# Kernel tuning notes

Measured on AMD Instinct MI355X. Metric: run time of the kernel, lower is better.

The kernel has to match this reference:

```python
import jax, jax.numpy as jnp
import numpy as np

N_NODES = 65536
IN_FEAT = 512
OUT_FEAT = 256
N_REL = 3
N_EDGES = 500000
NEG_SLOPE = 0.2  # DGL GATConv default
EPS = 1e-9


def setup_inputs() -> dict:
    key = jax.random.key(0)
    ks = jax.random.split(key, 7)
    h = jax.random.normal(ks[0], (N_NODES, IN_FEAT), dtype=jnp.float32)
    # Glorot-ish scaling keeps attention logits in a sane range
    W = jax.random.normal(ks[1], (N_REL, IN_FEAT, OUT_FEAT), dtype=jnp.float32) / np.sqrt(IN_FEAT)
    attn_l = jax.random.normal(ks[2], (N_REL, OUT_FEAT), dtype=jnp.float32) / np.sqrt(OUT_FEAT)
    attn_r = jax.random.normal(ks[3], (N_REL, OUT_FEAT), dtype=jnp.float32) / np.sqrt(OUT_FEAT)
    b = jnp.zeros((N_REL, OUT_FEAT), dtype=jnp.float32)
    src = jax.random.randint(ks[4], (N_REL, N_EDGES), 0, N_NODES, dtype=jnp.int32)
    dst = jax.random.randint(ks[5], (N_REL, N_EDGES), 0, N_NODES, dtype=jnp.int32)
    return {"h": h, "W": W, "attn_l": attn_l, "attn_r": attn_r, "b": b, "src": src, "dst": dst}


def _gat_relation(h, W_r, al_r, ar_r, b_r, src_r, dst_r):
    n = h.shape[0]
    z = h @ W_r                                  # [N, F_out] dense projection
    el = z @ al_r                                # [N] per-node left logit
    er = z @ ar_r                                # [N] per-node right logit
    e = jax.nn.leaky_relu(el[src_r] + er[dst_r], NEG_SLOPE)  # [E]
    # edge_softmax over incoming edges of each destination node
    m = jax.ops.segment_max(e, dst_r, num_segments=n)        # [N]
    w = jnp.exp(e - m[dst_r])                                # [E]
    denom = jax.ops.segment_sum(w, dst_r, num_segments=n)    # [N]
    alpha = w / (denom[dst_r] + EPS)                         # [E]
    out = jax.ops.segment_sum(alpha[:, None] * z[src_r], dst_r, num_segments=n)
    return out + b_r


def reference(h, W, attn_l, attn_r, b, src, dst):
    n_rel = W.shape[0]
    out = jnp.zeros((h.shape[0], W.shape[2]), dtype=h.dtype)
    # HeteroGraphConv default aggregate='sum' over relations; num_heads=1 then squeeze
    for r in range(n_rel):
        out = out + _gat_relation(h, W[r], attn_l[r], attn_r[r], b[r], src[r], dst[r])
    return out
```

## Files before the change

### kernel.cpp

```cpp
#include <hip/hip_runtime.h>
#include <hip/hip_bf16.h>
#include <cstdint>
#include <cstddef>

#define N_NODES 65536
#define IN_FEAT 512
#define OUT_FEAT 256
#define N_REL 3
#define TOT_EDGES (N_REL * 500000)
#define N_EDGES 500000
#define NEG_SLOPE 0.2f
#define EPS_F 1e-9f
#define BK 64

typedef __bf16 bf16x8 __attribute__((ext_vector_type(8)));
typedef float f32x4 __attribute__((ext_vector_type(4)));

__device__ __forceinline__ void async16(const void* g, void* l) {
    __builtin_amdgcn_global_load_lds(
        (const __attribute__((address_space(1))) unsigned int*)g,
        (__attribute__((address_space(3))) unsigned int*)l, 16, 0, 0);
}

__global__ __launch_bounds__(256) void kPrep(
    const float* __restrict__ W, const float* __restrict__ h,
    __bf16* __restrict__ Wt, __bf16* __restrict__ hb,
    float* __restrict__ el, float* __restrict__ er, int* __restrict__ head,
    int useHb) {
    __shared__ float tile[64][65];
    const int b = blockIdx.x;
    const int t = threadIdx.x;
    if (b < 768) {
        int i = b * 256 + t;
        el[i] = 0.f;
        er[i] = 0.f;
        head[i] = -1;
    } else if (b < 864) {
        int b2 = b - 768;
        int r = b2 >> 5;
        int kt = (b2 >> 2) & 7;
        int nt = b2 & 3;
        int k0 = kt * 64, n0 = nt * 64;
        int trow = t >> 6, tcol = t & 63;
        const float* Wr = W + (size_t)r * IN_FEAT * OUT_FEAT;
#pragma unroll
        for (int p = 0; p < 16; p++) {
            int k = p * 4 + trow;
            tile[k][tcol] = Wr[(size_t)(k0 + k) * OUT_FEAT + n0 + tcol];
        }
        __syncthreads();
        __bf16* Wtr = Wt + (size_t)r * OUT_FEAT * IN_FEAT;
#pragma unroll
        for (int p = 0; p < 16; p++) {
            int n = p * 4 + trow;
            Wtr[(size_t)(n0 + n) * IN_FEAT + k0 + tcol] = (__bf16)tile[tcol][n];
        }
    } else if (useHb) {
        size_t i = (size_t)(b - 864) * 256 + t;
        const float4* src = (const float4*)h + i * 2;
        float4 v0 = src[0], v1 = src[1];
        bf16x8 w;
        w[0] = (__bf16)v0.x; w[1] = (__bf16)v0.y; w[2] = (__bf16)v0.z; w[3] = (__bf16)v0.w;
        w[4] = (__bf16)v1.x; w[5] = (__bf16)v1.y; w[6] = (__bf16)v1.z; w[7] = (__bf16)v1.w;
        *(bf16x8*)(hb + i * 8) = w;
    }
}

__global__ __launch_bounds__(256, 3) void kGemmA(
    const __bf16* __restrict__ hb, const __bf16* __restrict__ Wt,
    const float* __restrict__ attn_l, const float* __restrict__ attn_r,
    __bf16* __restrict__ z, float* __restrict__ el, float* __restrict__ er) {
    __shared__ __bf16 Al[128 * BK];
    __shared__ __bf16 Bl[128 * BK];
    const int r = blockIdx.z;
    const int t = threadIdx.x;
    const int lane = t & 63;
    const int wave = t >> 6;
    const int wm = wave >> 1, wn = wave & 1;
    const int colL = lane & 15, quad = lane >> 4;
    const int m_base = blockIdx.y * 128;
    const int n_base = blockIdx.x * 128;

    const __bf16* WtR = Wt + (size_t)r * OUT_FEAT * IN_FEAT + (size_t)n_base * IN_FEAT;

    f32x4 acc[4][4];
#pragma unroll
    for (int mt = 0; mt < 4; mt++)
#pragma unroll
        for (int nt = 0; nt < 4; nt++) acc[mt][nt] = (f32x4){0.f, 0.f, 0.f, 0.f};

    for (int k0 = 0; k0 < IN_FEAT; k0 += BK) {
        if (k0) __syncthreads();
#pragma unroll
        for (int i = 0; i < 4; i++) {
            int s = i * 256 + t;
            int n = s >> 3, cp = s & 7, cs = cp ^ (n & 7);
            const __bf16* g = WtR + (size_t)n * IN_FEAT + k0 + cs * 8;
            __bf16* l = Bl + (size_t)(i * 256 + (wave << 6)) * 8;
            async16(g, l);
        }
#pragma unroll
        for (int i = 0; i < 4; i++) {
            int s = i * 256 + t;
            int row = s >> 3, cp = s & 7, cs = cp ^ (row & 7);
            const __bf16* g = hb + (size_t)(m_base + row) * IN_FEAT + k0 + cs * 8;
            __bf16* l = Al + (size_t)(i * 256 + (wave << 6)) * 8;
            async16(g, l);
        }
        __syncthreads();
#pragma unroll
        for (int kk = 0; kk < 2; kk++) {
            const int cbase = kk * 4 + quad;
            bf16x8 af[4], bfr[4];
#pragma unroll
            for (int mt = 0; mt < 4; mt++) {
                int row = wm * 64 + mt * 16 + colL;
                int cp = cbase ^ (row & 7);
                af[mt] = *(const bf16x8*)(Al + (size_t)((row << 3) + cp) * 8);
            }
#pragma unroll
            for (int nt = 0; nt < 4; nt++) {
                int n = wn * 64 + nt * 16 + colL;
                int cp = cbase ^ (n & 7);
                bfr[nt] = *(const bf16x8*)(Bl + (size_t)((n << 3) + cp) * 8);
            }
#pragma unroll
            for (int mt = 0; mt < 4; mt++)
#pragma unroll
                for (int nt = 0; nt < 4; nt++)
                    acc[mt][nt] = __builtin_amdgcn_mfma_f32_16x16x32_bf16(
                        af[mt], bfr[nt], acc[mt][nt], 0, 0, 0);
        }
    }

    const float* alv = attn_l + r * OUT_FEAT;
    const float* arv = attn_r + r * OUT_FEAT;
    __bf16* zr = z + (size_t)r * N_NODES * OUT_FEAT;
    float elp[4][4], erp[4][4];
#pragma unroll
    for (int mt = 0; mt < 4; mt++)
#pragma unroll
        for (int q = 0; q < 4; q++) { elp[mt][q] = 0.f; erp[mt][q] = 0.f; }
#pragma unroll
    for (int mt = 0; mt < 4; mt++) {
#pragma unroll
        for (int nt = 0; nt < 4; nt++) {
            int c = n_base + wn * 64 + nt * 16 + colL;
            float al = alv[c], ar = arv[c];
#pragma unroll
            for (int q = 0; q < 4; q++) {
                float v = acc[mt][nt][q];
                int row = m_base + wm * 64 + mt * 16 + quad * 4 + q;
                zr[(size_t)row * OUT_FEAT + c] = (__bf16)v;
                elp[mt][q] += v * al;
                erp[mt][q] += v * ar;
            }
        }
    }
#pragma unroll
    for (int mt = 0; mt < 4; mt++)
#pragma unroll
        for (int q = 0; q < 4; q++) {
#pragma unroll
            for (int off = 1; off < 16; off <<= 1) {
                elp[mt][q] += __shfl_xor(elp[mt][q], off, 64);
                erp[mt][q] += __shfl_xor(erp[mt][q], off, 64);
            }
        }
    if (colL == 0) {
#pragma unroll
        for (int mt = 0; mt < 4; mt++)
#pragma unroll
            for (int q = 0; q < 4; q++) {
                int row = m_base + wm * 64 + mt * 16 + quad * 4 + q;
                atomicAdd(el + r * N_NODES + row, elp[mt][q]);
                atomicAdd(er + r * N_NODES + row, erp[mt][q]);
            }
    }
}

__global__ __launch_bounds__(256) void kGemmC(
    const float* __restrict__ h, const __bf16* __restrict__ Wt,
    const float* __restrict__ attn_l, const float* __restrict__ attn_r,
    __bf16* __restrict__ z, float* __restrict__ el, float* __restrict__ er) {
    __shared__ __bf16 Al[128 * BK];
    __shared__ __bf16 Bl[256 * BK];
    const int r = blockIdx.y;
    const int t = threadIdx.x;
    const int lane = t & 63;
    const int wave = t >> 6;
    const int wm = wave >> 1, wn = wave & 1;
    const int colL = lane & 15, quad = lane >> 4;
    const int m_base = blockIdx.x * 128;
    const __bf16* WtR = Wt + (size_t)r * OUT_FEAT * IN_FEAT;

    f32x4 acc[4][8];
#pragma unroll
    for (int mt = 0; mt < 4; mt++)
#pragma unroll
        for (int nt = 0; nt < 8; nt++) acc[mt][nt] = (f32x4){0.f, 0.f, 0.f, 0.f};

    for (int k0 = 0; k0 < IN_FEAT; k0 += BK) {
        if (k0) __syncthreads();
#pragma unroll
        for (int i = 0; i < 8; i++) {
            int s = i * 256 + t;
            int n = s >> 3, cp = s & 7, cs = cp ^ (n & 7);
            const __bf16* g = WtR + (size_t)n * IN_FEAT + k0 + cs * 8;
            __bf16* l = Bl + (size_t)(i * 256 + (wave << 6)) * 8;
            async16(g, l);
        }
#pragma unroll
        for (int i = 0; i < 4; i++) {
            int s = i * 256 + t;
            int row = s >> 3, cp = s & 7, cs = cp ^ (row & 7);
            const float* g = h + (size_t)(m_base + row) * IN_FEAT + k0 + cs * 8;
            float4 v0 = ((const float4*)g)[0];
            float4 v1 = ((const float4*)g)[1];
            bf16x8 w;
            w[0] = (__bf16)v0.x; w[1] = (__bf16)v0.y; w[2] = (__bf16)v0.z; w[3] = (__bf16)v0.w;
            w[4] = (__bf16)v1.x; w[5] = (__bf16)v1.y; w[6] = (__bf16)v1.z; w[7] = (__bf16)v1.w;
            *(bf16x8*)(Al + (size_t)s * 8) = w;
        }
        __syncthreads();
#pragma unroll
        for (int kk = 0; kk < 2; kk++) {
            const int cbase = kk * 4 + quad;
            bf16x8 af[4], bfr[8];
#pragma unroll
            for (int mt = 0; mt < 4; mt++) {
                int row = wm * 64 + mt * 16 + colL;
                int cp = cbase ^ (row & 7);
                af[mt] = *(const bf16x8*)(Al + (size_t)((row << 3) + cp) * 8);
            }
#pragma unroll
            for (int nt = 0; nt < 8; nt++) {
                int n = wn * 128 + nt * 16 + colL;
                int cp = cbase ^ (n & 7);
                bfr[nt] = *(const bf16x8*)(Bl + (size_t)((n << 3) + cp) * 8);
            }
#pragma unroll
            for (int mt = 0; mt < 4; mt++)
#pragma unroll
                for (int nt = 0; nt < 8; nt++)
                    acc[mt][nt] = __builtin_amdgcn_mfma_f32_16x16x32_bf16(
                        af[mt], bfr[nt], acc[mt][nt], 0, 0, 0);
        }
    }
    const float* alv = attn_l + r * OUT_FEAT;
    const float* arv = attn_r + r * OUT_FEAT;
    __bf16* zr = z + (size_t)r * N_NODES * OUT_FEAT;
    float elp[4][4], erp[4][4];
#pragma unroll
    for (int mt = 0; mt < 4; mt++)
#pragma unroll
        for (int q = 0; q < 4; q++) { elp[mt][q] = 0.f; erp[mt][q] = 0.f; }
#pragma unroll
    for (int mt = 0; mt < 4; mt++) {
#pragma unroll
        for (int nt = 0; nt < 8; nt++) {
            int c = wn * 128 + nt * 16 + colL;
            float al = alv[c], ar = arv[c];
#pragma unroll
            for (int q = 0; q < 4; q++) {
                float v = acc[mt][nt][q];
                int row = m_base + wm * 64 + mt * 16 + quad * 4 + q;
                zr[(size_t)row * OUT_FEAT + c] = (__bf16)v;
                elp[mt][q] += v * al;
                erp[mt][q] += v * ar;
            }
        }
    }
#pragma unroll
    for (int mt = 0; mt < 4; mt++)
#pragma unroll
        for (int q = 0; q < 4; q++) {
#pragma unroll
            for (int off = 1; off < 16; off <<= 1) {
                elp[mt][q] += __shfl_xor(elp[mt][q], off, 64);
                erp[mt][q] += __shfl_xor(erp[mt][q], off, 64);
            }
        }
    if (colL == 0) {
#pragma unroll
        for (int mt = 0; mt < 4; mt++)
#pragma unroll
            for (int q = 0; q < 4; q++) {
                int row = m_base + wm * 64 + mt * 16 + quad * 4 + q;
                atomicAdd(el + r * N_NODES + row, elp[mt][q]);
                atomicAdd(er + r * N_NODES + row, erp[mt][q]);
            }
    }
}

__global__ void kLink(const int* __restrict__ dst, const int* __restrict__ srcArr,
                      int* __restrict__ head, int2* __restrict__ next2) {
    int i = blockIdx.x * blockDim.x + threadIdx.x;
    if (i >= TOT_EDGES) return;
    int r = i / N_EDGES;
    int d = dst[i];
    int prev = atomicExch(head + r * N_NODES + d, i);
    next2[i] = make_int2(prev, srcArr[i]);
}

__global__ __launch_bounds__(192) void kAgg(
    const __bf16* __restrict__ z, const int* __restrict__ head,
    const int2* __restrict__ next2,
    const float* __restrict__ el, const float* __restrict__ er,
    const float* __restrict__ bias, float* __restrict__ out) {
    __shared__ float cm[6][256];
    const int t = threadIdx.x;
    const int wv = t >> 6;
    const int lane = t & 63;
    const int half = lane >> 5;
    const int l = lane & 31;
    const int hw = wv * 2 + half;
    const int nl = (hw >= 3) ? 1 : 0;
    const int r = hw - nl * 3;
    const int node = blockIdx.x * 2 + nl;
    const int idx = r * N_NODES + node;

    const float erv = er[idx];
    const float* elr = el + r * N_NODES;
    const uint4* zrel = (const uint4*)(z + (size_t)r * N_NODES * OUT_FEAT);

    float p0 = 0.f, p1 = 0.f, p2 = 0.f, p3 = 0.f;
    float p4 = 0.f, p5 = 0.f, p6 = 0.f, p7 = 0.f;
    float wsum = 0.f;
    int cur = head[idx];
    while (cur >= 0) {
        int2 ns = next2[cur];
        int s = ns.y;
        float x = elr[s] + erv;
        x = x > 0.f ? x : NEG_SLOPE * x;
        float w = __expf(x);
        uint4 v = zrel[(size_t)s * 32 + l];
        wsum += w;
        p0 += w * __uint_as_float(v.x << 16);
        p1 += w * __uint_as_float(v.x & 0xFFFF0000u);
        p2 += w * __uint_as_float(v.y << 16);
        p3 += w * __uint_as_float(v.y & 0xFFFF0000u);
        p4 += w * __uint_as_float(v.z << 16);
        p5 += w * __uint_as_float(v.z & 0xFFFF0000u);
        p6 += w * __uint_as_float(v.w << 16);
        p7 += w * __uint_as_float(v.w & 0xFFFF0000u);
        cur = ns.x;
    }
    float invd = 1.f / (wsum + EPS_F);
    float* cr = &cm[hw][l * 8];
    *(float4*)cr       = make_float4(p0 * invd, p1 * invd, p2 * invd, p3 * invd);
    *(float4*)(cr + 4) = make_float4(p4 * invd, p5 * invd, p6 * invd, p7 * invd);
    __syncthreads();

    if (r == 0) {
        const int c = l * 8;
        const float* r0 = &cm[nl * 3 + 0][c];
        const float* r1 = &cm[nl * 3 + 1][c];
        const float* r2 = &cm[nl * 3 + 2][c];
        const float* b0 = bias + c;
        const float* b1 = bias + OUT_FEAT + c;
        const float* b2 = bias + 2 * OUT_FEAT + c;
        float f0 = r0[0] + r1[0] + r2[0] + b0[0] + b1[0] + b2[0];
        float f1 = r0[1] + r1[1] + r2[1] + b0[1] + b1[1] + b2[1];
        float f2 = r0[2] + r1[2] + r2[2] + b0[2] + b1[2] + b2[2];
        float f3 = r0[3] + r1[3] + r2[3] + b0[3] + b1[3] + b2[3];
        float f4 = r0[4] + r1[4] + r2[4] + b0[4] + b1[4] + b2[4];
        float f5 = r0[5] + r1[5] + r2[5] + b0[5] + b1[5] + b2[5];
        float f6 = r0[6] + r1[6] + r2[6] + b0[6] + b1[6] + b2[6];
        float f7 = r0[7] + r1[7] + r2[7] + b0[7] + b1[7] + b2[7];
        float* orow = out + (size_t)node * OUT_FEAT + c;
        *(float4*)orow       = make_float4(f0, f1, f2, f3);
        *(float4*)(orow + 4) = make_float4(f4, f5, f6, f7);
    }
}

extern "C" void kernel_launch(void* const* d_in, const int* in_sizes, int n_in,
                              void* d_out, int out_size, void* d_ws, size_t ws_size,
                              hipStream_t stream) {
    const float* h      = (const float*)d_in[0];
    const float* W      = (const float*)d_in[1];
    const float* attn_l = (const float*)d_in[2];
    const float* attn_r = (const float*)d_in[3];
    const float* bias   = (const float*)d_in[4];
    const int*   src    = (const int*)d_in[5];
    const int*   dst    = (const int*)d_in[6];
    float* out = (float*)d_out;
    char* ws = (char*)d_ws;

    const bool useHb = ws_size >= (size_t)190000000;
    size_t off_b = 0;
    auto alloc = [&](size_t bytes) {
        size_t o = off_b;
        off_b = (off_b + bytes + 255) & ~(size_t)255;
        return o;
    };
    size_t oZ    = alloc((size_t)N_REL * N_NODES * OUT_FEAT * 2);
    size_t oHB   = useHb ? alloc((size_t)N_NODES * IN_FEAT * 2) : 0;
    size_t oWT   = alloc((size_t)N_REL * OUT_FEAT * IN_FEAT * 2);
    size_t oEL   = alloc((size_t)N_REL * N_NODES * 4);
    size_t oER   = alloc((size_t)N_REL * N_NODES * 4);
    size_t oHEAD = alloc((size_t)N_REL * N_NODES * 4);
    size_t oNEXT = alloc((size_t)TOT_EDGES * 8);

    __bf16* z    = (__bf16*)(ws + oZ);
    __bf16* hb   = (__bf16*)(ws + oHB);
    __bf16* Wt   = (__bf16*)(ws + oWT);
    float*  el   = (float*)(ws + oEL);
    float*  er   = (float*)(ws + oER);
    int*    head = (int*)(ws + oHEAD);
    int2*   next2 = (int2*)(ws + oNEXT);

    kPrep<<<17248, 256, 0, stream>>>(W, h, Wt, hb, el, er, head, useHb ? 1 : 0);
    kLink<<<(TOT_EDGES + 255) / 256, 256, 0, stream>>>(dst, src, head, next2);
    if (useHb) {
        kGemmA<<<dim3(2, 512, 3), 256, 0, stream>>>(hb, Wt, attn_l, attn_r, z, el, er);
    } else {
        kGemmC<<<dim3(N_NODES / 128, N_REL), 256, 0, stream>>>(h, Wt, attn_l, attn_r, z, el, er);
    }
    kAgg<<<N_NODES / 2, 192, 0, stream>>>(z, head, next2, el, er, bias, out);
}
```

Measured before the change: 527.5 us.

## Drop bf16 h staging, XCD-aware GEMM scheduling, and interleave two node chains in aggregation

Removes the separate fp32-to-bf16 conversion pass over h and always uses the full-N GEMM that reads fp32 h directly. Blocks are remapped so each XCD handles a contiguous band of rows across all three relations, so the same h rows are shared in cache. The aggregation kernel now walks two destination nodes' linked lists at once per half-wave, giving more independent memory loads in flight to hide gather latency. The cost is more registers and divergence in the aggregation loop and an fp32 load-and-convert path inside the GEMM.

```diff
diff --git a/kernel.cpp b/kernel.cpp
--- a/kernel.cpp
+++ b/kernel.cpp
@@ -23,10 +23,9 @@
 }
 
 __global__ __launch_bounds__(256) void kPrep(
-    const float* __restrict__ W, const float* __restrict__ h,
-    __bf16* __restrict__ Wt, __bf16* __restrict__ hb,
-    float* __restrict__ el, float* __restrict__ er, int* __restrict__ head,
-    int useHb) {
+    const float* __restrict__ W,
+    __bf16* __restrict__ Wt,
+    float* __restrict__ el, float* __restrict__ er, int* __restrict__ head) {
     __shared__ float tile[64][65];
     const int b = blockIdx.x;
     const int t = threadIdx.x;
@@ -35,7 +34,7 @@
         el[i] = 0.f;
         er[i] = 0.f;
         head[i] = -1;
-    } else if (b < 864) {
+    } else {
         int b2 = b - 768;
         int r = b2 >> 5;
         int kt = (b2 >> 2) & 7;
@@ -55,143 +54,28 @@
             int n = p * 4 + trow;
             Wtr[(size_t)(n0 + n) * IN_FEAT + k0 + tcol] = (__bf16)tile[tcol][n];
         }
-    } else if (useHb) {
-        size_t i = (size_t)(b - 864) * 256 + t;
-        const float4* src = (const float4*)h + i * 2;
-        float4 v0 = src[0], v1 = src[1];
-        bf16x8 w;
-        w[0] = (__bf16)v0.x; w[1] = (__bf16)v0.y; w[2] = (__bf16)v0.z; w[3] = (__bf16)v0.w;
-        w[4] = (__bf16)v1.x; w[5] = (__bf16)v1.y; w[6] = (__bf16)v1.z; w[7] = (__bf16)v1.w;
-        *(bf16x8*)(hb + i * 8) = w;
-    }
-}
-
-__global__ __launch_bounds__(256, 3) void kGemmA(
-    const __bf16* __restrict__ hb, const __bf16* __restrict__ Wt,
+    }
+}
+
+__global__ __launch_bounds__(256, 2) void kGemm(
+    const float* __restrict__ h, const __bf16* __restrict__ Wt,
     const float* __restrict__ attn_l, const float* __restrict__ attn_r,
     __bf16* __restrict__ z, float* __restrict__ el, float* __restrict__ er) {
     __shared__ __bf16 Al[128 * BK];
-    __shared__ __bf16 Bl[128 * BK];
-    const int r = blockIdx.z;
+    __shared__ __bf16 Bl[256 * BK];
+    const int bid = blockIdx.x;
+    const int xcd = bid & 7;
+    const int slot = bid >> 3;
+    const int mt6 = slot / 3;
+    const int r = slot - mt6 * 3;
+    const int m_base = (xcd * 64 + mt6) * 128;
+
     const int t = threadIdx.x;
     const int lane = t & 63;
     const int wave = t >> 6;
     const int wm = wave >> 1, wn = wave & 1;
     const int colL = lane & 15, quad = lane >> 4;
-    const int m_base = blockIdx.y * 128;
-    const int n_base = blockIdx.x * 128;
-
-    const __bf16* WtR = Wt + (size_t)r * OUT_FEAT * IN_FEAT + (size_t)n_base * IN_FEAT;
-
-    f32x4 acc[4][4];
-#pragma unroll
-    for (int mt = 0; mt < 4; mt++)
-#pragma unroll
-        for (int nt = 0; nt < 4; nt++) acc[mt][nt] = (f32x4){0.f, 0.f, 0.f, 0.f};
-
-    for (int k0 = 0; k0 < IN_FEAT; k0 += BK) {
-        if (k0) __syncthreads();
-#pragma unroll
-        for (int i = 0; i < 4; i++) {
-            int s = i * 256 + t;
-            int n = s >> 3, cp = s & 7, cs = cp ^ (n & 7);
-            const __bf16* g = WtR + (size_t)n * IN_FEAT + k0 + cs * 8;
-            __bf16* l = Bl + (size_t)(i * 256 + (wave << 6)) * 8;
-            async16(g, l);
-        }
-#pragma unroll
-        for (int i = 0; i < 4; i++) {
-            int s = i * 256 + t;
-            int row = s >> 3, cp = s & 7, cs = cp ^ (row & 7);
-            const __bf16* g = hb + (size_t)(m_base + row) * IN_FEAT + k0 + cs * 8;
-            __bf16* l = Al + (size_t)(i * 256 + (wave << 6)) * 8;
-            async16(g, l);
-        }
-        __syncthreads();
-#pragma unroll
-        for (int kk = 0; kk < 2; kk++) {
-            const int cbase = kk * 4 + quad;
-            bf16x8 af[4], bfr[4];
-#pragma unroll
-            for (int mt = 0; mt < 4; mt++) {
-                int row = wm * 64 + mt * 16 + colL;
-                int cp = cbase ^ (row & 7);
-                af[mt] = *(const bf16x8*)(Al + (size_t)((row << 3) + cp) * 8);
-            }
-#pragma unroll
-            for (int nt = 0; nt < 4; nt++) {
-                int n = wn * 64 + nt * 16 + colL;
-                int cp = cbase ^ (n & 7);
-                bfr[nt] = *(const bf16x8*)(Bl + (size_t)((n << 3) + cp) * 8);
-            }
-#pragma unroll
-            for (int mt = 0; mt < 4; mt++)
-#pragma unroll
-                for (int nt = 0; nt < 4; nt++)
-                    acc[mt][nt] = __builtin_amdgcn_mfma_f32_16x16x32_bf16(
-                        af[mt], bfr[nt], acc[mt][nt], 0, 0, 0);
-        }
-    }
-
-    const float* alv = attn_l + r * OUT_FEAT;
-    const float* arv = attn_r + r * OUT_FEAT;
-    __bf16* zr = z + (size_t)r * N_NODES * OUT_FEAT;
-    float elp[4][4], erp[4][4];
-#pragma unroll
-    for (int mt = 0; mt < 4; mt++)
-#pragma unroll
-        for (int q = 0; q < 4; q++) { elp[mt][q] = 0.f; erp[mt][q] = 0.f; }
-#pragma unroll
-    for (int mt = 0; mt < 4; mt++) {
-#pragma unroll
-        for (int nt = 0; nt < 4; nt++) {
-            int c = n_base + wn * 64 + nt * 16 + colL;
-            float al = alv[c], ar = arv[c];
-#pragma unroll
-            for (int q = 0; q < 4; q++) {
-                float v = acc[mt][nt][q];
-                int row = m_base + wm * 64 + mt * 16 + quad * 4 + q;
-                zr[(size_t)row * OUT_FEAT + c] = (__bf16)v;
-                elp[mt][q] += v * al;
-                erp[mt][q] += v * ar;
-            }
-        }
-    }
-#pragma unroll
-    for (int mt = 0; mt < 4; mt++)
-#pragma unroll
-        for (int q = 0; q < 4; q++) {
-#pragma unroll
-            for (int off = 1; off < 16; off <<= 1) {
-                elp[mt][q] += __shfl_xor(elp[mt][q], off, 64);
-                erp[mt][q] += __shfl_xor(erp[mt][q], off, 64);
-            }
-        }
-    if (colL == 0) {
-#pragma unroll
-        for (int mt = 0; mt < 4; mt++)
-#pragma unroll
-            for (int q = 0; q < 4; q++) {
-                int row = m_base + wm * 64 + mt * 16 + quad * 4 + q;
-                atomicAdd(el + r * N_NODES + row, elp[mt][q]);
-                atomicAdd(er + r * N_NODES + row, erp[mt][q]);
-            }
-    }
-}
-
-__global__ __launch_bounds__(256) void kGemmC(
-    const float* __restrict__ h, const __bf16* __restrict__ Wt,
-    const float* __restrict__ attn_l, const float* __restrict__ attn_r,
-    __bf16* __restrict__ z, float* __restrict__ el, float* __restrict__ er) {
-    __shared__ __bf16 Al[128 * BK];
-    __shared__ __bf16 Bl[256 * BK];
-    const int r = blockIdx.y;
-    const int t = threadIdx.x;
-    const int lane = t & 63;
-    const int wave = t >> 6;
-    const int wm = wave >> 1, wn = wave & 1;
-    const int colL = lane & 15, quad = lane >> 4;
-    const int m_base = blockIdx.x * 128;
+
     const __bf16* WtR = Wt + (size_t)r * OUT_FEAT * IN_FEAT;
 
     f32x4 acc[4][8];
@@ -247,6 +131,7 @@
                         af[mt], bfr[nt], acc[mt][nt], 0, 0, 0);
         }
     }
+
     const float* alv = attn_l + r * OUT_FEAT;
     const float* arv = attn_r + r * OUT_FEAT;
     __bf16* zr = z + (size_t)r * N_NODES * OUT_FEAT;
@@ -308,7 +193,7 @@
     const int2* __restrict__ next2,
     const float* __restrict__ el, const float* __restrict__ er,
     const float* __restrict__ bias, float* __restrict__ out) {
-    __shared__ float cm[6][256];
+    __shared__ float cm[12][256];
     const int t = threadIdx.x;
     const int wv = t >> 6;
     const int lane = t & 63;
@@ -317,57 +202,94 @@
     const int hw = wv * 2 + half;
     const int nl = (hw >= 3) ? 1 : 0;
     const int r = hw - nl * 3;
-    const int node = blockIdx.x * 2 + nl;
-    const int idx = r * N_NODES + node;
-
-    const float erv = er[idx];
+    const int nodeA = blockIdx.x * 4 + nl;
+    const int nodeB = nodeA + 2;
+    const int idxA = r * N_NODES + nodeA;
+    const int idxB = r * N_NODES + nodeB;
+
+    const float ervA = er[idxA];
+    const float ervB = er[idxB];
     const float* elr = el + r * N_NODES;
     const uint4* zrel = (const uint4*)(z + (size_t)r * N_NODES * OUT_FEAT);
 
-    float p0 = 0.f, p1 = 0.f, p2 = 0.f, p3 = 0.f;
-    float p4 = 0.f, p5 = 0.f, p6 = 0.f, p7 = 0.f;
-    float wsum = 0.f;
-    int cur = head[idx];
-    while (cur >= 0) {
-        int2 ns = next2[cur];
-        int s = ns.y;
-        float x = elr[s] + erv;
-        x = x > 0.f ? x : NEG_SLOPE * x;
-        float w = __expf(x);
-        uint4 v = zrel[(size_t)s * 32 + l];
-        wsum += w;
-        p0 += w * __uint_as_float(v.x << 16);
-        p1 += w * __uint_as_float(v.x & 0xFFFF0000u);
-        p2 += w * __uint_as_float(v.y << 16);
-        p3 += w * __uint_as_float(v.y & 0xFFFF0000u);
-        p4 += w * __uint_as_float(v.z << 16);
-        p5 += w * __uint_as_float(v.z & 0xFFFF0000u);
-        p6 += w * __uint_as_float(v.w << 16);
-        p7 += w * __uint_as_float(v.w & 0xFFFF0000u);
-        cur = ns.x;
-    }
-    float invd = 1.f / (wsum + EPS_F);
-    float* cr = &cm[hw][l * 8];
-    *(float4*)cr       = make_float4(p0 * invd, p1 * invd, p2 * invd, p3 * invd);
-    *(float4*)(cr + 4) = make_float4(p4 * invd, p5 * invd, p6 * invd, p7 * invd);
+    float a0 = 0.f, a1 = 0.f, a2 = 0.f, a3 = 0.f;
+    float a4 = 0.f, a5 = 0.f, a6 = 0.f, a7 = 0.f;
+    float b0 = 0.f, b1 = 0.f, b2 = 0.f, b3 = 0.f;
+    float b4 = 0.f, b5 = 0.f, b6 = 0.f, b7 = 0.f;
+    float wsumA = 0.f, wsumB = 0.f;
+    int curA = head[idxA];
+    int curB = head[idxB];
+    while (curA >= 0 || curB >= 0) {
+        int2 nsA, nsB;
+        const bool doA = curA >= 0, doB = curB >= 0;
+        if (doA) nsA = next2[curA];
+        if (doB) nsB = next2[curB];
+        if (doA) {
+            int s = nsA.y;
+            float x = elr[s] + ervA;
+            x = x > 0.f ? x : NEG_SLOPE * x;
+            float w = __expf(x);
+            uint4 v = zrel[(size_t)s * 32 + l];
+            wsumA += w;
+            a0 += w * __uint_as_float(v.x << 16);
+            a1 += w * __uint_as_float(v.x & 0xFFFF0000u);
+            a2 += w * __uint_as_float(v.y << 16);
+            a3 += w * __uint_as_float(v.y & 0xFFFF0000u);
+            a4 += w * __uint_as_float(v.z << 16);
+            a5 += w * __uint_as_float(v.z & 0xFFFF0000u);
+            a6 += w * __uint_as_float(v.w << 16);
+            a7 += w * __uint_as_float(v.w & 0xFFFF0000u);
+            curA = nsA.x;
+        }
+        if (doB) {
+            int s = nsB.y;
+            float x = elr[s] + ervB;
+            x = x > 0.f ? x : NEG_SLOPE * x;
+            float w = __expf(x);
+            uint4 v = zrel[(size_t)s * 32 + l];
+            wsumB += w;
+            b0 += w * __uint_as_float(v.x << 16);
+            b1 += w * __uint_as_float(v.x & 0xFFFF0000u);
+            b2 += w * __uint_as_float(v.y << 16);
+            b3 += w * __uint_as_float(v.y & 0xFFFF0000u);
+            b4 += w * __uint_as_float(v.z << 16);
+            b5 += w * __uint_as_float(v.z & 0xFFFF0000u);
+            b6 += w * __uint_as_float(v.w << 16);
+            b7 += w * __uint_as_float(v.w & 0xFFFF0000u);
+            curB = nsB.x;
+        }
+    }
+    {
+        float invd = 1.f / (wsumA + EPS_F);
+        float* cr = &cm[hw][l * 8];
+        *(float4*)cr       = make_float4(a0 * invd, a1 * invd, a2 * invd, a3 * invd);
+        *(float4*)(cr + 4) = make_float4(a4 * invd, a5 * invd, a6 * invd, a7 * invd);
+    }
+    {
+        float invd = 1.f / (wsumB + EPS_F);
+        float* cr = &cm[6 + hw][l * 8];
+        *(float4*)cr       = make_float4(b0 * invd, b1 * invd, b2 * invd, b3 * invd);
+        *(float4*)(cr + 4) = make_float4(b4 * invd, b5 * invd, b6 * invd, b7 * invd);
+    }
     __syncthreads();
 
-    if (r == 0) {
+    if (hw < 4) {
         const int c = l * 8;
-        const float* r0 = &cm[nl * 3 + 0][c];
-        const float* r1 = &cm[nl * 3 + 1][c];
-        const float* r2 = &cm[nl * 3 + 2][c];
-        const float* b0 = bias + c;
-        const float* b1 = bias + OUT_FEAT + c;
-        const float* b2 = bias + 2 * OUT_FEAT + c;
-        float f0 = r0[0] + r1[0] + r2[0] + b0[0] + b1[0] + b2[0];
-        float f1 = r0[1] + r1[1] + r2[1] + b0[1] + b1[1] + b2[1];
-        float f2 = r0[2] + r1[2] + r2[2] + b0[2] + b1[2] + b2[2];
-        float f3 = r0[3] + r1[3] + r2[3] + b0[3] + b1[3] + b2[3];
-        float f4 = r0[4] + r1[4] + r2[4] + b0[4] + b1[4] + b2[4];
-        float f5 = r0[5] + r1[5] + r2[5] + b0[5] + b1[5] + b2[5];
-        float f6 = r0[6] + r1[6] + r2[6] + b0[6] + b1[6] + b2[6];
-        float f7 = r0[7] + r1[7] + r2[7] + b0[7] + b1[7] + b2[7];
+        const float* r0 = &cm[hw * 3 + 0][c];
+        const float* r1 = &cm[hw * 3 + 1][c];
+        const float* r2 = &cm[hw * 3 + 2][c];
+        const float* q0 = bias + c;
+        const float* q1 = bias + OUT_FEAT + c;
+        const float* q2 = bias + 2 * OUT_FEAT + c;
+        float f0 = r0[0] + r1[0] + r2[0] + q0[0] + q1[0] + q2[0];
+        float f1 = r0[1] + r1[1] + r2[1] + q0[1] + q1[1] + q2[1];
+        float f2 = r0[2] + r1[2] + r2[2] + q0[2] + q1[2] + q2[2];
+        float f3 = r0[3] + r1[3] + r2[3] + q0[3] + q1[3] + q2[3];
+        float f4 = r0[4] + r1[4] + r2[4] + q0[4] + q1[4] + q2[4];
+        float f5 = r0[5] + r1[5] + r2[5] + q0[5] + q1[5] + q2[5];
+        float f6 = r0[6] + r1[6] + r2[6] + q0[6] + q1[6] + q2[6];
+        float f7 = r0[7] + r1[7] + r2[7] + q0[7] + q1[7] + q2[7];
+        const int node = blockIdx.x * 4 + hw;
         float* orow = out + (size_t)node * OUT_FEAT + c;
         *(float4*)orow       = make_float4(f0, f1, f2, f3);
         *(float4*)(orow + 4) = make_float4(f4, f5, f6, f7);
@@ -387,7 +309,6 @@
     float* out = (float*)d_out;
     char* ws = (char*)d_ws;
 
-    const bool useHb = ws_size >= (size_t)190000000;
     size_t off_b = 0;
     auto alloc = [&](size_t bytes) {
         size_t o = off_b;
@@ -395,27 +316,21 @@
         return o;
     };
     size_t oZ    = alloc((size_t)N_REL * N_NODES * OUT_FEAT * 2);
-    size_t oHB   = useHb ? alloc((size_t)N_NODES * IN_FEAT * 2) : 0;
     size_t oWT   = alloc((size_t)N_REL * OUT_FEAT * IN_FEAT * 2);
     size_t oEL   = alloc((size_t)N_REL * N_NODES * 4);
     size_t oER   = alloc((size_t)N_REL * N_NODES * 4);
     size_t oHEAD = alloc((size_t)N_REL * N_NODES * 4);
     size_t oNEXT = alloc((size_t)TOT_EDGES * 8);
 
-    __bf16* z    = (__bf16*)(ws + oZ);
-    __bf16* hb   = (__bf16*)(ws + oHB);
-    __bf16* Wt   = (__bf16*)(ws + oWT);
-    float*  el   = (float*)(ws + oEL);
-    float*  er   = (float*)(ws + oER);
-    int*    head = (int*)(ws + oHEAD);
+    __bf16* z     = (__bf16*)(ws + oZ);
+    __bf16* Wt    = (__bf16*)(ws + oWT);
+    float*  el    = (float*)(ws + oEL);
+    float*  er    = (float*)(ws + oER);
+    int*    head  = (int*)(ws + oHEAD);
     int2*   next2 = (int2*)(ws + oNEXT);
 
-    kPrep<<<17248, 256, 0, stream>>>(W, h, Wt, hb, el, er, head, useHb ? 1 : 0);
+    kPrep<<<864, 256, 0, stream>>>(W, Wt, el, er, head);
     kLink<<<(TOT_EDGES + 255) / 256, 256, 0, stream>>>(dst, src, head, next2);
-    if (useHb) {
-        kGemmA<<<dim3(2, 512, 3), 256, 0, stream>>>(hb, Wt, attn_l, attn_r, z, el, er);
-    } else {
-        kGemmC<<<dim3(N_NODES / 128, N_REL), 256, 0, stream>>>(h, Wt, attn_l, attn_r, z, el, er);
-    }
-    kAgg<<<N_NODES / 2, 192, 0, stream>>>(z, head, next2, el, er, bias, out);
-}
+    kGemm<<<1536, 256, 0, stream>>>(h, Wt, attn_l, attn_r, z, el, er);
+    kAgg<<<N_NODES / 4, 192, 0, stream>>>(z, head, next2, el, er, bias, out);
+}
```

After: 495.4 us. 6.1% less time.
